# Performance work log

Measured on AMD Instinct MI355X. Metric: run time of the kernel, lower is better.

Reference implementation:

```python
import jax, jax.numpy as jnp
import numpy as np

EMBED = 1536
HEADS = 12
EPS = 1e-5


def _layernorm(x, gamma, beta):
    mu = x.mean(axis=-1, keepdims=True)
    var = ((x - mu) ** 2).mean(axis=-1, keepdims=True)
    return (x - mu) * jax.lax.rsqrt(var + EPS) * gamma + beta


def setup_inputs() -> dict:
    key = jax.random.key(0)
    ks = jax.random.split(key, 8)
    N, L, E = 8, 2048, EMBED
    x = jax.random.normal(ks[0], (N, L, E), dtype=jnp.float32)
    s = 0.02
    Wv = jax.random.normal(ks[1], (E, E), dtype=jnp.float32) * s
    Wk = jax.random.normal(ks[2], (E, E), dtype=jnp.float32) * s
    Wq = jax.random.normal(ks[3], (E, E), dtype=jnp.float32) * s
    Wo = jax.random.normal(ks[4], (E, E), dtype=jnp.float32) * s
    bo = jnp.zeros((E,), dtype=jnp.float32)
    gamma = jnp.ones((E,), dtype=jnp.float32)
    beta = jnp.zeros((E,), dtype=jnp.float32)
    return {"combined_embeddings": x, "Wv": Wv, "Wk": Wk, "Wq": Wq,
            "Wo": Wo, "bo": bo, "gamma": gamma, "beta": beta}


def reference(combined_embeddings, Wv, Wk, Wq, Wo, bo, gamma, beta):
    x = combined_embeddings
    N, L, E = x.shape
    H, hd = HEADS, E // HEADS
    # projections (torch Linear: x @ W^T), reshape to (N, H, L, hd)
    v = (x @ Wv.T).reshape(N, L, H, hd).transpose(0, 2, 1, 3)
    k = (x @ Wk.T).reshape(N, L, H, hd).transpose(0, 2, 1, 3)
    q = (x @ Wq.T).reshape(N, L, H, hd).transpose(0, 2, 1, 3)
    # NOTE: faithful to the source, einsum labels treat axis1 (heads) as q/k
    # and axis2 (sequence) as h -> heads-over-heads attention per position.
    energy = jnp.einsum('nqhd,nkhd->nhqk', q, k)  # (N, L, H, H)
    attention = jax.nn.softmax(energy / jnp.sqrt(jnp.float32(E)), axis=3)
    out = jnp.einsum('nhql,nlhd->nqhd', attention, v)  # (N, H, L, hd)
    out = out.transpose(0, 2, 1, 3).reshape(N, L, E)
    out = out @ Wo.T + bo
    out = _layernorm(out + x, gamma, beta)
    # small extra attention
    e_actions = out[:, 2:][None]          # (1, N, L-2, E)
    e_state = out.mean(axis=1)[None]      # (1, N, E)
    scores = jnp.matmul(e_state, jnp.swapaxes(e_actions, -2, -1))
    scores = scores / jnp.sqrt(jnp.float32(E))   # (1, N, N, L-2)
    weights = jax.nn.softmax(scores, axis=-1)
    attended = jnp.matmul(weights, e_actions)    # (1, N, N, E)
    return attended, weights
```

## Files before the change

kernel.cpp:

```cpp
#include <hip/hip_runtime.h>
#include <stdint.h>

typedef unsigned short u16;
typedef __bf16 bf16_t;
typedef bf16_t bf16x8 __attribute__((ext_vector_type(8)));
typedef float f32x4 __attribute__((ext_vector_type(4)));

#define E_DIM 1536
#define N_B 8
#define L_SEQ 2048
#define NT 2046
#define SCALE 0.025515518f
#define LN_EPS 1e-5f
#define NTILES 24
#define NXV 6291456
#define NWV 589824

__device__ __forceinline__ u16 f2b(float f) {
  union { float f; uint32_t u; } v; v.f = f;
  uint32_t u = v.u + 0x7FFFu + ((v.u >> 16) & 1u);
  return (u16)(u >> 16);
}
__device__ __forceinline__ float b2f(u16 h) {
  union { uint32_t u; float f; } v; v.u = ((uint32_t)h) << 16; return v.f;
}

__device__ __forceinline__ void gload16(const u16* g, const bf16_t* l) {
  __builtin_amdgcn_global_load_lds((const __attribute__((address_space(1))) void*)g,
                                   (__attribute__((address_space(3))) void*)l,
                                   16, 0, 0);
}

#define BAR()   __builtin_amdgcn_s_barrier()
#define SCHB()  __builtin_amdgcn_sched_barrier(0)
#define VM4()   asm volatile("s_waitcnt vmcnt(4)" ::: "memory")
#define VM0()   asm volatile("s_waitcnt vmcnt(0)" ::: "memory")

__global__ void cvt_all(const float* __restrict__ x,  const float* __restrict__ Wq,
                        const float* __restrict__ Wk, const float* __restrict__ Wv,
                        const float* __restrict__ Wo,
                        u16* __restrict__ xb,  u16* __restrict__ wqb,
                        u16* __restrict__ wkb, u16* __restrict__ wvb,
                        u16* __restrict__ wob)
{
  int i = blockIdx.x * 256 + threadIdx.x;
  const float* src; u16* dst; int o;
  if (i < NXV)              { src = x;  dst = xb;  o = i; }
  else if (i < NXV + NWV)   { src = Wq; dst = wqb; o = i - NXV; }
  else if (i < NXV + 2*NWV) { src = Wk; dst = wkb; o = i - NXV - NWV; }
  else if (i < NXV + 3*NWV) { src = Wv; dst = wvb; o = i - NXV - 2*NWV; }
  else                      { src = Wo; dst = wob; o = i - NXV - 3*NWV; }
  float4 f = ((const float4*)src)[o];
  ushort4 u;
  u.x = f2b(f.x); u.y = f2b(f.y); u.z = f2b(f.z); u.w = f2b(f.w);
  ((ushort4*)dst)[o] = u;
}

template<int FUSED>
__launch_bounds__(512, 2)
__global__ void gemm2c(const u16* __restrict__ Ag,
                       const u16* __restrict__ B0w, const u16* __restrict__ B1w,
                       const u16* __restrict__ B2w,
                       u16* __restrict__ C0, u16* __restrict__ C1, u16* __restrict__ C2,
                       const float* __restrict__ bias, const u16* __restrict__ resid16)
{
  extern __shared__ __attribute__((aligned(16))) bf16_t lds[];

  const int flat = (blockIdx.z * gridDim.y + blockIdx.y) * gridDim.x + blockIdx.x;
  const int xcd = flat & 7, bb_ = flat >> 3;
  const int gl = bb_ / 24, jj = bb_ % 24;
  const int g = gl * 8 + xcd;
  const int zz = g >> 4;
  const int gy = g & 15;
  const int tx = jj >> 2;
  const int ty = gy * 4 + (jj & 3);
  const int rowA = ty * 256, colB = tx * 256;

  const u16* Bg; u16* Cb;
  if (zz == 0)      { Bg = B0w; Cb = C0; }
  else if (zz == 1) { Bg = B1w; Cb = C1; }
  else              { Bg = B2w; Cb = C2; }

  const int tid = threadIdx.x;
  const int w = tid >> 6, lane = tid & 63;
  const int wr = w >> 2, wc = w & 3;

  const int rl = lane & 15, lsl = lane >> 4;
  const int sw8 = (lsl ^ ((rl >> 1) & 3)) * 8;
  const int arow = (wr * 128 + rl) * 32 + sw8;
  const int brow = (wc * 64 + rl) * 32 + sw8;

  const int r0s = tid >> 2, sps = tid & 3;
  const int sws = (sps ^ ((r0s >> 1) & 3)) * 8;
  const size_t sA0 = (size_t)(rowA + r0s) * E_DIM + sws;
  const size_t sA1 = (size_t)(rowA + 128 + r0s) * E_DIM + sws;
  const size_t sB0 = (size_t)(colB + r0s) * E_DIM + sws;
  const size_t sB1 = (size_t)(colB + 128 + r0s) * E_DIM + sws;
  const int wb0 = w * 512, wb1 = 4096 + w * 512;

  f32x4 acc[8][4];
#pragma unroll
  for (int m = 0; m < 8; ++m)
#pragma unroll
    for (int n = 0; n < 4; ++n)
#pragma unroll
      for (int q = 0; q < 4; ++q) acc[m][n][q] = 0.0f;

  gload16(Ag + sA0,      lds + 0     + wb0);  gload16(Ag + sA1,      lds + 0     + wb1);
  gload16(Bg + sB0,      lds + 32768 + wb0);  gload16(Bg + sB1,      lds + 32768 + wb1);
  gload16(Ag + sA0 + 32, lds + 8192  + wb0);  gload16(Ag + sA1 + 32, lds + 8192  + wb1);
  gload16(Bg + sB0 + 32, lds + 40960 + wb0);  gload16(Bg + sB1 + 32, lds + 40960 + wb1);
  gload16(Ag + sA0 + 64, lds + 16384 + wb0);  gload16(Ag + sA1 + 64, lds + 16384 + wb1);
  gload16(Bg + sB0 + 64, lds + 49152 + wb0);  gload16(Bg + sB1 + 64, lds + 49152 + wb1);
  VM4();
  BAR();

  bf16x8 a0[8], b0[4], a1[8], b1[4];
#pragma unroll
  for (int m = 0; m < 8; ++m) a0[m] = *(const bf16x8*)&lds[0 + arow + m * 512];
#pragma unroll
  for (int n = 0; n < 4; ++n) b0[n] = *(const bf16x8*)&lds[32768 + brow + n * 512];

  for (int t = 0; t < NTILES; ++t) {
    const int cur = t & 1, nxt = cur ^ 1;
    const int Ak1 = (cur * 2 + 1) * 8192, Bk1 = 32768 + (cur * 2 + 1) * 8192;
    const int AkN0 = nxt * 2 * 8192,      BkN0 = 32768 + nxt * 2 * 8192;
    const int AkN1 = (nxt * 2 + 1) * 8192, BkN1 = 32768 + (nxt * 2 + 1) * 8192;

#pragma unroll
    for (int m = 0; m < 8; ++m) a1[m] = *(const bf16x8*)&lds[Ak1 + arow + m * 512];
#pragma unroll
    for (int n = 0; n < 4; ++n) b1[n] = *(const bf16x8*)&lds[Bk1 + brow + n * 512];
    if (t + 1 < NTILES) {
      const size_t ko = (size_t)(t + 1) * 64 + 32;
      gload16(Ag + sA0 + ko, lds + AkN1 + wb0);  gload16(Ag + sA1 + ko, lds + AkN1 + wb1);
      gload16(Bg + sB0 + ko, lds + BkN1 + wb0);  gload16(Bg + sB1 + ko, lds + BkN1 + wb1);
    }
    SCHB();
    __builtin_amdgcn_s_setprio(1);
#pragma unroll
    for (int m = 0; m < 8; ++m)
#pragma unroll
      for (int n = 0; n < 4; ++n)
        acc[m][n] = __builtin_amdgcn_mfma_f32_16x16x32_bf16(a0[m], b0[n], acc[m][n], 0, 0, 0);
    __builtin_amdgcn_s_setprio(0);
    SCHB();
    if (t + 1 < NTILES) { VM4(); }
    BAR();

    if (t + 2 < NTILES) {
      const size_t ko = (size_t)(t + 2) * 64;
      gload16(Ag + sA0 + ko, lds + cur * 2 * 8192 + wb0);
      gload16(Ag + sA1 + ko, lds + cur * 2 * 8192 + wb1);
      gload16(Bg + sB0 + ko, lds + 32768 + cur * 2 * 8192 + wb0);
      gload16(Bg + sB1 + ko, lds + 32768 + cur * 2 * 8192 + wb1);
    }
    if (t + 1 < NTILES) {
#pragma unroll
      for (int m = 0; m < 8; ++m) a0[m] = *(const bf16x8*)&lds[AkN0 + arow + m * 512];
#pragma unroll
      for (int n = 0; n < 4; ++n) b0[n] = *(const bf16x8*)&lds[BkN0 + brow + n * 512];
    }
    SCHB();
    __builtin_amdgcn_s_setprio(1);
#pragma unroll
    for (int m = 0; m < 8; ++m)
#pragma unroll
      for (int n = 0; n < 4; ++n)
        acc[m][n] = __builtin_amdgcn_mfma_f32_16x16x32_bf16(a1[m], b1[n], acc[m][n], 0, 0, 0);
    __builtin_amdgcn_s_setprio(0);
    SCHB();
    if (t + 2 < NTILES)      { VM4(); }
    else if (t + 1 < NTILES) { VM0(); }
    BAR();
  }

  const int r0 = (lane >> 4) * 4;
#pragma unroll
  for (int m = 0; m < 8; ++m) {
#pragma unroll
    for (int n = 0; n < 4; ++n) {
      const int gcol = colB + wc * 64 + n * 16 + rl;
#pragma unroll
      for (int q = 0; q < 4; ++q) {
        const int grow = rowA + wr * 128 + m * 16 + r0 + q;
        const size_t idx = (size_t)grow * E_DIM + gcol;
        if (FUSED == 2)
          Cb[idx] = f2b(acc[m][n][q] + bias[gcol] + b2f(resid16[idx]));
        else
          Cb[idx] = f2b(acc[m][n][q]);
      }
    }
  }
}

__launch_bounds__(256)
__global__ void headmix(const u16* __restrict__ qb, const u16* __restrict__ kb,
                        const u16* __restrict__ vb, u16* __restrict__ aob)
{
  __shared__ float qs[12 * 132], ks2[12 * 132], vs[12 * 132];
  __shared__ float att[12][12];
  const int tid = threadIdx.x;
  const size_t base = (size_t)blockIdx.x * E_DIM;

  if (tid < 192) {
    const int i = tid >> 4, d0 = (tid & 15) * 8, p = i * 132 + d0;
    uint4 q4 = *(const uint4*)(qb + base + tid * 8);
    uint4 k4 = *(const uint4*)(kb + base + tid * 8);
    uint4 v4 = *(const uint4*)(vb + base + tid * 8);
#pragma unroll
    for (int c = 0; c < 4; ++c) {
      uint32_t qa = (&q4.x)[c], ka = (&k4.x)[c], va = (&v4.x)[c];
      qs[p + 2*c]     = b2f((u16)(qa & 0xFFFF));
      qs[p + 2*c + 1] = b2f((u16)(qa >> 16));
      ks2[p + 2*c]     = b2f((u16)(ka & 0xFFFF));
      ks2[p + 2*c + 1] = b2f((u16)(ka >> 16));
      vs[p + 2*c]     = b2f((u16)(va & 0xFFFF));
      vs[p + 2*c + 1] = b2f((u16)(va >> 16));
    }
  }
  __syncthreads();

  if (tid < 144) {
    int i = tid / 12, j = tid % 12;
    const float4* qr = (const float4*)&qs[i * 132];
    const float4* kr = (const float4*)&ks2[j * 132];
    float s = 0.f;
#pragma unroll 8
    for (int d4 = 0; d4 < 32; ++d4) {
      float4 a = qr[d4], b = kr[d4];
      s += a.x * b.x + a.y * b.y + a.z * b.z + a.w * b.w;
    }
    att[i][j] = s * SCALE;
  }
  __syncthreads();

  if (tid < 12) {
    float mx = att[tid][0];
#pragma unroll
    for (int j = 1; j < 12; ++j) mx = fmaxf(mx, att[tid][j]);
    float ev[12], sum = 0.f;
#pragma unroll
    for (int j = 0; j < 12; ++j) { ev[j] = expf(att[tid][j] - mx); sum += ev[j]; }
    float inv = 1.f / sum;
#pragma unroll
    for (int j = 0; j < 12; ++j) att[tid][j] = ev[j] * inv;
  }
  __syncthreads();

  for (int e = tid; e < E_DIM; e += 256) {
    int i = e >> 7, d = e & 127;
    float o = 0.f;
#pragma unroll
    for (int j = 0; j < 12; ++j) o += att[i][j] * vs[j * 132 + d];
    aob[base + e] = f2b(o);
  }
}

__launch_bounds__(256)
__global__ void ln_kernel(const u16* __restrict__ p, u16* __restrict__ ho,
                          const float* __restrict__ gamma, const float* __restrict__ beta)
{
  __shared__ float rs[4], rq[4];
  __shared__ float mean_s, rstd_s;
  const int tid = threadIdx.x, w = tid >> 6, lane = tid & 63;
  const uint32_t* row = (const uint32_t*)(p + (size_t)blockIdx.x * E_DIM);
  uint32_t* orow = (uint32_t*)(ho + (size_t)blockIdx.x * E_DIM);

  float v[6], s = 0.f, sq = 0.f;
#pragma unroll
  for (int i = 0; i < 3; ++i) {
    uint32_t u = row[tid + i * 256];
    float lo = b2f((u16)(u & 0xFFFF)), hi = b2f((u16)(u >> 16));
    v[2*i] = lo; v[2*i+1] = hi;
    s += lo + hi; sq += lo * lo + hi * hi;
  }
#pragma unroll
  for (int off = 32; off > 0; off >>= 1) {
    s  += __shfl_down(s, off);
    sq += __shfl_down(sq, off);
  }
  if (lane == 0) { rs[w] = s; rq[w] = sq; }
  __syncthreads();
  if (tid == 0) {
    float S = rs[0] + rs[1] + rs[2] + rs[3];
    float Q = rq[0] + rq[1] + rq[2] + rq[3];
    float mu = S * (1.f / 1536.f);
    float var = Q * (1.f / 1536.f) - mu * mu;
    mean_s = mu; rstd_s = rsqrtf(var + LN_EPS);
  }
  __syncthreads();
  const float mu = mean_s, rstd = rstd_s;
#pragma unroll
  for (int i = 0; i < 3; ++i) {
    int j = tid + i * 256;
    float o0 = (v[2*i]   - mu) * rstd * gamma[2*j]   + beta[2*j];
    float o1 = (v[2*i+1] - mu) * rstd * gamma[2*j+1] + beta[2*j+1];
    orow[j] = (uint32_t)f2b(o0) | ((uint32_t)f2b(o1) << 16);
  }
}

__launch_bounds__(256)
__global__ void estate_partial(const u16* __restrict__ outp, float* __restrict__ part)
{
  const int tid = threadIdx.x;
  const int b = blockIdx.x, rc = blockIdx.y;
  if (tid >= 192) return;
  const uint4* base = (const uint4*)(outp + ((size_t)b * L_SEQ + rc * 64) * E_DIM);
  float a[8];
#pragma unroll
  for (int k = 0; k < 8; ++k) a[k] = 0.f;
  for (int r = 0; r < 64; ++r) {
    uint4 v = base[(size_t)r * 192 + tid];
#pragma unroll
    for (int c = 0; c < 4; ++c) {
      uint32_t u = (&v.x)[c];
      a[2*c]   += b2f((u16)(u & 0xFFFF));
      a[2*c+1] += b2f((u16)(u >> 16));
    }
  }
  float* dst = part + ((size_t)rc * N_B + b) * E_DIM + tid * 8;
#pragma unroll
  for (int k = 0; k < 8; ++k) dst[k] = a[k];
}
__global__ void estate_reduce(const float* __restrict__ part, float* __restrict__ est)
{
  const int i = blockIdx.x * 256 + threadIdx.x;
  if (i < N_B * E_DIM) {
    float s = 0.f;
#pragma unroll
    for (int z = 0; z < 32; ++z) s += part[(size_t)z * N_B * E_DIM + i];
    est[i] = s * (1.f / 2048.f);
  }
}

__launch_bounds__(256)
__global__ void scores_kernel(const u16* __restrict__ outp, const float* __restrict__ est,
                              float* __restrict__ wout)
{
  __shared__ float es[N_B * E_DIM];
  const int tid = threadIdx.x, wv = tid >> 6, lane = tid & 63;
  const int b = blockIdx.y;
  for (int i = tid; i < N_B * E_DIM; i += 256) es[i] = est[i];
  __syncthreads();

  for (int ti = 0; ti < 16; ++ti) {
    int t = blockIdx.x * 64 + wv * 16 + ti;
    if (t >= NT) continue;
    const uint32_t* row =
        (const uint32_t*)(outp + ((size_t)b * L_SEQ + 2 + t) * E_DIM);
    float a[8];
#pragma unroll
    for (int s = 0; s < 8; ++s) a[s] = 0.f;
    for (int c = 0; c < 12; ++c) {
      uint32_t pv = row[c * 64 + lane];
      float v0 = b2f((u16)(pv & 0xFFFF)), v1 = b2f((u16)(pv >> 16));
      int idx = (c * 64 + lane) * 2;
#pragma unroll
      for (int s = 0; s < 8; ++s)
        a[s] += es[s * E_DIM + idx] * v0 + es[s * E_DIM + idx + 1] * v1;
    }
#pragma unroll
    for (int off = 32; off > 0; off >>= 1)
#pragma unroll
      for (int s = 0; s < 8; ++s) a[s] += __shfl_down(a[s], off);
    if (lane == 0) {
#pragma unroll
      for (int s = 0; s < 8; ++s)
        wout[(size_t)(b * N_B + s) * NT + t] = a[s] * SCALE;
    }
  }
}

__launch_bounds__(256)
__global__ void softmax_w(float* __restrict__ wbase)
{
  float* p = wbase + (size_t)blockIdx.x * NT;
  __shared__ float r1[4], r2[4];
  __shared__ float bmax, bsum;
  const int tid = threadIdx.x, wv = tid >> 6, lane = tid & 63;

  float vals[8], mx = -1e30f;
#pragma unroll
  for (int i = 0; i < 8; ++i) {
    int t = tid + i * 256;
    vals[i] = (t < NT) ? p[t] : -1e30f;
    mx = fmaxf(mx, vals[i]);
  }
#pragma unroll
  for (int off = 32; off > 0; off >>= 1) mx = fmaxf(mx, __shfl_down(mx, off));
  if (lane == 0) r1[wv] = mx;
  __syncthreads();
  if (tid == 0) bmax = fmaxf(fmaxf(r1[0], r1[1]), fmaxf(r1[2], r1[3]));
  __syncthreads();
  mx = bmax;

  float sum = 0.f;
#pragma unroll
  for (int i = 0; i < 8; ++i) {
    int t = tid + i * 256;
    if (t < NT) { vals[i] = expf(vals[i] - mx); sum += vals[i]; }
  }
#pragma unroll
  for (int off = 32; off > 0; off >>= 1) sum += __shfl_down(sum, off);
  if (lane == 0) r2[wv] = sum;
  __syncthreads();
  if (tid == 0) bsum = r2[0] + r2[1] + r2[2] + r2[3];
  __syncthreads();
  const float inv = 1.f / bsum;
#pragma unroll
  for (int i = 0; i < 8; ++i) {
    int t = tid + i * 256;
    if (t < NT) p[t] = vals[i] * inv;
  }
}

__launch_bounds__(256)
__global__ void attended_partial(const u16* __restrict__ outp, const float* __restrict__ wts,
                                 float* __restrict__ part)
{
  __shared__ float wl[8][64];
  const int tid = threadIdx.x;
  const int b = blockIdx.x, tc = blockIdx.y;
  const int t0 = tc * 64;
  const int cnt = (NT - t0 < 64) ? (NT - t0) : 64;

  for (int i = tid; i < 8 * 64; i += 256) {
    int s = i >> 6, tt = i & 63;
    wl[s][tt] = (tt < cnt) ? wts[(size_t)(b * N_B + s) * NT + t0 + tt] : 0.f;
  }
  __syncthreads();
  if (tid >= 192) return;

  const uint4* base = (const uint4*)(outp + ((size_t)b * L_SEQ + 2 + t0) * E_DIM);
  float a[8][8];
#pragma unroll
  for (int s = 0; s < 8; ++s)
#pragma unroll
    for (int k = 0; k < 8; ++k) a[s][k] = 0.f;

  for (int tt = 0; tt < cnt; ++tt) {
    uint4 v = base[(size_t)tt * 192 + tid];
    float e[8];
#pragma unroll
    for (int c = 0; c < 4; ++c) {
      uint32_t u = (&v.x)[c];
      e[2*c]   = b2f((u16)(u & 0xFFFF));
      e[2*c+1] = b2f((u16)(u >> 16));
    }
#pragma unroll
    for (int s = 0; s < 8; ++s) {
      const float wv = wl[s][tt];
#pragma unroll
      for (int k = 0; k < 8; ++k) a[s][k] += wv * e[k];
    }
  }
#pragma unroll
  for (int s = 0; s < 8; ++s) {
    float* dst = part + (((size_t)tc * N_B + b) * N_B + s) * E_DIM + tid * 8;
#pragma unroll
    for (int k = 0; k < 8; ++k) dst[k] = a[s][k];
  }
}
__global__ void attended_reduce(const float* __restrict__ part, float* __restrict__ outp)
{
  const int i = blockIdx.x * 256 + threadIdx.x;
  float s = 0.f;
#pragma unroll
  for (int z = 0; z < 32; ++z) s += part[(size_t)z * N_B * N_B * E_DIM + i];
  outp[i] = s;
}

extern "C" void kernel_launch(void* const* d_in, const int* in_sizes, int n_in,
                              void* d_out, int out_size, void* d_ws, size_t ws_size,
                              hipStream_t stream)
{
  (void)in_sizes; (void)n_in; (void)out_size; (void)ws_size;
  const float* x     = (const float*)d_in[0];
  const float* Wv    = (const float*)d_in[1];
  const float* Wk    = (const float*)d_in[2];
  const float* Wq    = (const float*)d_in[3];
  const float* Wo    = (const float*)d_in[4];
  const float* bo    = (const float*)d_in[5];
  const float* gamma = (const float*)d_in[6];
  const float* beta  = (const float*)d_in[7];
  float* out = (float*)d_out;

  char* ws = (char*)d_ws;
  size_t off = 0;
  auto alloc = [&](size_t bytes) -> void* {
    void* p = ws + off;
    off += (bytes + 255) & ~(size_t)255;
    return p;
  };
  const size_t ME = (size_t)16384 * E_DIM;
  const size_t WE = (size_t)E_DIM * E_DIM;
  u16*   xb     = (u16*)alloc(ME * 2);
  u16*   wqb    = (u16*)alloc(WE * 2);
  u16*   wkb    = (u16*)alloc(WE * 2);
  u16*   wvb    = (u16*)alloc(WE * 2);
  u16*   wob    = (u16*)alloc(WE * 2);
  u16*   qb     = (u16*)alloc(ME * 2);
  u16*   kb     = (u16*)alloc(ME * 2);
  u16*   vb     = (u16*)alloc(ME * 2);
  u16*   aob    = (u16*)alloc(ME * 2);
  u16*   lnbufh = (u16*)alloc(ME * 2);
  float* est    = (float*)alloc((size_t)N_B * E_DIM * 4);
  float* estp   = (float*)alloc((size_t)32 * N_B * E_DIM * 4);
  float* attp   = (float*)alloc((size_t)32 * N_B * N_B * E_DIM * 4);

  float* wout = out + 98304;

  hipFuncSetAttribute(reinterpret_cast<const void*>(gemm2c<0>),
                      hipFuncAttributeMaxDynamicSharedMemorySize, 131072);
  hipFuncSetAttribute(reinterpret_cast<const void*>(gemm2c<2>),
                      hipFuncAttributeMaxDynamicSharedMemorySize, 131072);

  cvt_all<<<dim3((NXV + 4 * NWV) / 256), 256, 0, stream>>>(
      x, Wq, Wk, Wv, Wo, xb, wqb, wkb, wvb, wob);

  gemm2c<0><<<dim3(6, 64, 3), 512, 131072, stream>>>(
      xb, wqb, wkb, wvb, qb, kb, vb, nullptr, nullptr);

  headmix<<<dim3(16384), 256, 0, stream>>>(qb, kb, vb, aob);

  gemm2c<2><<<dim3(6, 64, 1), 512, 131072, stream>>>(
      aob, wob, wob, wob, lnbufh, lnbufh, lnbufh, bo, xb);

  u16* lnh = aob;
  ln_kernel<<<dim3(16384), 256, 0, stream>>>(lnbufh, lnh, gamma, beta);

  estate_partial<<<dim3(8, 32), 256, 0, stream>>>(lnh, estp);
  estate_reduce<<<dim3(48), 256, 0, stream>>>(estp, est);

  scores_kernel<<<dim3(32, 8), 256, 0, stream>>>(lnh, est, wout);
  softmax_w<<<dim3(64), 256, 0, stream>>>(wout);

  attended_partial<<<dim3(8, 32), 256, 0, stream>>>(lnh, wout, attp);
  attended_reduce<<<dim3(384), 256, 0, stream>>>(attp, out);
}
```

Before: 492.0 us.

## Fuse layernorm with e_state partial sums and vectorize headmix output

Merges the layernorm kernel and the estate_partial column-sum kernel, so each single-wave block normalizes 8 rows with a shuffle-only reduction and accumulates per-column partial sums. This removes a full re-read of the normalized activations and one kernel launch. The headmix epilogue is also rewritten to compute 8 outputs per thread using float4 shared-memory reads and a single 16-byte store. In exchange, the partial-sum buffer grows from 32 to 256 slices, so estate_reduce sums many more partials, and the LN blocks now run only 64 threads.

```diff
diff --git a/kernel.cpp b/kernel.cpp
--- a/kernel.cpp
+++ b/kernel.cpp
@@ -248,88 +248,97 @@
   }
   __syncthreads();
 
-  for (int e = tid; e < E_DIM; e += 256) {
-    int i = e >> 7, d = e & 127;
-    float o = 0.f;
-#pragma unroll
-    for (int j = 0; j < 12; ++j) o += att[i][j] * vs[j * 132 + d];
-    aob[base + e] = f2b(o);
-  }
-}
-
-__launch_bounds__(256)
-__global__ void ln_kernel(const u16* __restrict__ p, u16* __restrict__ ho,
-                          const float* __restrict__ gamma, const float* __restrict__ beta)
-{
-  __shared__ float rs[4], rq[4];
-  __shared__ float mean_s, rstd_s;
-  const int tid = threadIdx.x, w = tid >> 6, lane = tid & 63;
-  const uint32_t* row = (const uint32_t*)(p + (size_t)blockIdx.x * E_DIM);
-  uint32_t* orow = (uint32_t*)(ho + (size_t)blockIdx.x * E_DIM);
-
-  float v[6], s = 0.f, sq = 0.f;
-#pragma unroll
-  for (int i = 0; i < 3; ++i) {
-    uint32_t u = row[tid + i * 256];
-    float lo = b2f((u16)(u & 0xFFFF)), hi = b2f((u16)(u >> 16));
-    v[2*i] = lo; v[2*i+1] = hi;
-    s += lo + hi; sq += lo * lo + hi * hi;
-  }
-#pragma unroll
-  for (int off = 32; off > 0; off >>= 1) {
-    s  += __shfl_down(s, off);
-    sq += __shfl_down(sq, off);
-  }
-  if (lane == 0) { rs[w] = s; rq[w] = sq; }
-  __syncthreads();
-  if (tid == 0) {
-    float S = rs[0] + rs[1] + rs[2] + rs[3];
-    float Q = rq[0] + rq[1] + rq[2] + rq[3];
-    float mu = S * (1.f / 1536.f);
-    float var = Q * (1.f / 1536.f) - mu * mu;
-    mean_s = mu; rstd_s = rsqrtf(var + LN_EPS);
-  }
-  __syncthreads();
-  const float mu = mean_s, rstd = rstd_s;
-#pragma unroll
-  for (int i = 0; i < 3; ++i) {
-    int j = tid + i * 256;
-    float o0 = (v[2*i]   - mu) * rstd * gamma[2*j]   + beta[2*j];
-    float o1 = (v[2*i+1] - mu) * rstd * gamma[2*j+1] + beta[2*j+1];
-    orow[j] = (uint32_t)f2b(o0) | ((uint32_t)f2b(o1) << 16);
-  }
-}
-
-__launch_bounds__(256)
-__global__ void estate_partial(const u16* __restrict__ outp, float* __restrict__ part)
-{
-  const int tid = threadIdx.x;
-  const int b = blockIdx.x, rc = blockIdx.y;
-  if (tid >= 192) return;
-  const uint4* base = (const uint4*)(outp + ((size_t)b * L_SEQ + rc * 64) * E_DIM);
-  float a[8];
-#pragma unroll
-  for (int k = 0; k < 8; ++k) a[k] = 0.f;
-  for (int r = 0; r < 64; ++r) {
-    uint4 v = base[(size_t)r * 192 + tid];
-#pragma unroll
-    for (int c = 0; c < 4; ++c) {
-      uint32_t u = (&v.x)[c];
-      a[2*c]   += b2f((u16)(u & 0xFFFF));
-      a[2*c+1] += b2f((u16)(u >> 16));
-    }
-  }
-  float* dst = part + ((size_t)rc * N_B + b) * E_DIM + tid * 8;
-#pragma unroll
-  for (int k = 0; k < 8; ++k) dst[k] = a[k];
+  if (tid < 192) {
+    const int i = tid >> 4, d0 = (tid & 15) * 8;
+    float o[8];
+#pragma unroll
+    for (int k = 0; k < 8; ++k) o[k] = 0.f;
+#pragma unroll
+    for (int j = 0; j < 12; ++j) {
+      const float aij = att[i][j];
+      const float4 v0 = *(const float4*)&vs[j * 132 + d0];
+      const float4 v1 = *(const float4*)&vs[j * 132 + d0 + 4];
+      o[0] += aij * v0.x; o[1] += aij * v0.y; o[2] += aij * v0.z; o[3] += aij * v0.w;
+      o[4] += aij * v1.x; o[5] += aij * v1.y; o[6] += aij * v1.z; o[7] += aij * v1.w;
+    }
+    uint4 u;
+#pragma unroll
+    for (int c = 0; c < 4; ++c)
+      (&u.x)[c] = (uint32_t)f2b(o[2*c]) | ((uint32_t)f2b(o[2*c+1]) << 16);
+    *(uint4*)(aob + base + tid * 8) = u;
+  }
+}
+
+__launch_bounds__(64)
+__global__ void ln_estate(const u16* __restrict__ p, u16* __restrict__ ho,
+                          const float* __restrict__ gamma, const float* __restrict__ beta,
+                          float* __restrict__ estp)
+{
+  const int lane = threadIdx.x;
+  const int b = blockIdx.x, ch = blockIdx.y;
+  const size_t row0 = (size_t)b * L_SEQ + ch * 8;
+
+  float ga[24], be[24];
+#pragma unroll
+  for (int j = 0; j < 3; ++j)
+#pragma unroll
+    for (int k = 0; k < 8; ++k) {
+      ga[j*8+k] = gamma[j*512 + lane*8 + k];
+      be[j*8+k] = beta [j*512 + lane*8 + k];
+    }
+
+  float acc[24];
+#pragma unroll
+  for (int k = 0; k < 24; ++k) acc[k] = 0.f;
+
+  for (int r = 0; r < 8; ++r) {
+    const uint4* row = (const uint4*)(p + (row0 + r) * E_DIM);
+    uint4* orow = (uint4*)(ho + (row0 + r) * E_DIM);
+    float v[24], s = 0.f, sq = 0.f;
+#pragma unroll
+    for (int j = 0; j < 3; ++j) {
+      uint4 u = row[j*64 + lane];
+#pragma unroll
+      for (int c = 0; c < 4; ++c) {
+        uint32_t w2 = (&u.x)[c];
+        float lo = b2f((u16)(w2 & 0xFFFF)), hi = b2f((u16)(w2 >> 16));
+        v[j*8+2*c] = lo; v[j*8+2*c+1] = hi;
+        s += lo + hi; sq += lo*lo + hi*hi;
+      }
+    }
+#pragma unroll
+    for (int off = 32; off > 0; off >>= 1) {
+      s  += __shfl_xor(s, off);
+      sq += __shfl_xor(sq, off);
+    }
+    const float mu = s * (1.f / 1536.f);
+    const float rstd = rsqrtf(sq * (1.f / 1536.f) - mu * mu + LN_EPS);
+#pragma unroll
+    for (int j = 0; j < 3; ++j) {
+      uint4 u;
+#pragma unroll
+      for (int c = 0; c < 4; ++c) {
+        float o0 = (v[j*8+2*c]   - mu) * rstd * ga[j*8+2*c]   + be[j*8+2*c];
+        float o1 = (v[j*8+2*c+1] - mu) * rstd * ga[j*8+2*c+1] + be[j*8+2*c+1];
+        acc[j*8+2*c] += o0; acc[j*8+2*c+1] += o1;
+        (&u.x)[c] = (uint32_t)f2b(o0) | ((uint32_t)f2b(o1) << 16);
+      }
+      orow[j*64 + lane] = u;
+    }
+  }
+  float* dst = estp + ((size_t)ch * N_B + b) * E_DIM;
+#pragma unroll
+  for (int j = 0; j < 3; ++j)
+#pragma unroll
+    for (int k = 0; k < 8; ++k)
+      dst[j*512 + lane*8 + k] = acc[j*8+k];
 }
 __global__ void estate_reduce(const float* __restrict__ part, float* __restrict__ est)
 {
   const int i = blockIdx.x * 256 + threadIdx.x;
   if (i < N_B * E_DIM) {
     float s = 0.f;
-#pragma unroll
-    for (int z = 0; z < 32; ++z) s += part[(size_t)z * N_B * E_DIM + i];
+    for (int z = 0; z < 256; ++z) s += part[(size_t)z * N_B * E_DIM + i];
     est[i] = s * (1.f / 2048.f);
   }
 }
@@ -506,7 +515,7 @@
   u16*   aob    = (u16*)alloc(ME * 2);
   u16*   lnbufh = (u16*)alloc(ME * 2);
   float* est    = (float*)alloc((size_t)N_B * E_DIM * 4);
-  float* estp   = (float*)alloc((size_t)32 * N_B * E_DIM * 4);
+  float* estp   = (float*)alloc((size_t)256 * N_B * E_DIM * 4);
   float* attp   = (float*)alloc((size_t)32 * N_B * N_B * E_DIM * 4);
 
   float* wout = out + 98304;
@@ -528,9 +537,7 @@
       aob, wob, wob, wob, lnbufh, lnbufh, lnbufh, bo, xb);
 
   u16* lnh = aob;
-  ln_kernel<<<dim3(16384), 256, 0, stream>>>(lnbufh, lnh, gamma, beta);
-
-  estate_partial<<<dim3(8, 32), 256, 0, stream>>>(lnh, estp);
+  ln_estate<<<dim3(8, 256), 64, 0, stream>>>(lnbufh, lnh, gamma, beta, estp);
   estate_reduce<<<dim3(48), 256, 0, stream>>>(estp, est);
 
   scores_kernel<<<dim3(32, 8), 256, 0, stream>>>(lnh, est, wout);
```

After: 496.4 us. About the same (+0.9%).
